# Kernel tuning notes

Hardware: AMD Instinct MI355X
Metric: run time of the kernel (lower is better)

The kernel has to match this reference:

```python
import jax, jax.numpy as jnp
import numpy as np

B, D_IN, D_OUT = 8192, 1024, 1024


def setup_inputs() -> dict:
    key = jax.random.key(0)
    k1, k2 = jax.random.split(key)
    x = jax.random.normal(k1, (B, D_IN), dtype=jnp.float32)
    # Keras add_weight(shape=(3, input_dim, output_dim), initializer='uniform')
    kernel = jax.random.normal(k2, (3, D_IN, D_OUT), dtype=jnp.float32) * 0.05
    return {"x": x, "kernel": kernel}


def reference(x, kernel):
    # x: (B, D). Layer does expand_dims(axis=1) -> (B, 1, D) (seq_len == 1).
    output_dim = kernel.shape[-1]
    xe = x[:, None, :]                                   # (B, 1, D)
    q = jnp.einsum('bsd,do->bso', xe, kernel[0])         # (B, 1, O)
    k = jnp.einsum('bsd,do->bso', xe, kernel[1])         # (B, 1, O)
    v = jnp.einsum('bsd,do->bso', xe, kernel[2])         # (B, 1, O)
    scores = jnp.einsum('bqo,bko->bqk', q, k) / jnp.sqrt(
        jnp.asarray(output_dim, x.dtype))                # (B, 1, 1)
    attn = jax.nn.softmax(scores, axis=-1)
    out = jnp.einsum('bqk,bko->bqo', attn, v)            # (B, 1, O)
    return out
```

## Files before the change

### kernel.cpp

```cpp
#include <hip/hip_runtime.h>
#include <hip/hip_bf16.h>
#include <stdint.h>

#define AS1 __attribute__((address_space(1)))
#define AS3 __attribute__((address_space(3)))

typedef __attribute__((ext_vector_type(8))) short bf16x8_t;
typedef __attribute__((ext_vector_type(4))) float f32x4_t;

#define DDIM 1024
#define WT_ELEMS ((size_t)DDIM * DDIM)

static __device__ inline ushort f32_to_bf16_rne(float f) {
  union { float f; uint32_t u; } v;
  v.f = f;
  v.u += 0x7FFFu + ((v.u >> 16) & 1u);
  return (ushort)(v.u >> 16);
}

__global__ __launch_bounds__(256) void transpose_w(const float* __restrict__ W,
                                                   ushort* __restrict__ Wt) {
  __shared__ float tile[64][65];
  const int t  = threadIdx.x;
  const int bk = blockIdx.x;
  const int bn = blockIdx.y;
#pragma unroll
  for (int s = 0; s < 4; ++s) {
    const int slot = (s << 8) + t;
    const int r    = slot >> 4;
    const int c4   = (slot & 15) << 2;
    const float4 v = *(const float4*)(W + (size_t)(bk * 64 + r) * DDIM + bn * 64 + c4);
    tile[r][c4 + 0] = v.x; tile[r][c4 + 1] = v.y;
    tile[r][c4 + 2] = v.z; tile[r][c4 + 3] = v.w;
  }
  __syncthreads();
#pragma unroll
  for (int s = 0; s < 2; ++s) {
    const int slot = (s << 8) + t;
    const int n    = slot >> 3;
    const int k8   = (slot & 7) << 3;
    union { ushort h[8]; uint4 u; } tmp;
#pragma unroll
    for (int j = 0; j < 8; ++j) tmp.h[j] = f32_to_bf16_rne(tile[k8 + j][n]);
    *(uint4*)(Wt + (size_t)(bn * 64 + n) * DDIM + bk * 64 + k8) = tmp.u;
  }
}

__global__ __launch_bounds__(256, 2) void gemm_fa(const float* __restrict__ X,
                                                  const ushort* __restrict__ Wt,
                                                  float* __restrict__ C) {
  __shared__ __align__(16) ushort As[2][128 * 64];
  __shared__ __align__(16) ushort Bs[2][128 * 64];

  const int t    = threadIdx.x;
  const int wave = t >> 6;
  const int lane = t & 63;
  const int m0 = blockIdx.x * 128;
  const int n0 = blockIdx.y * 128;

  const int sr = t >> 3;
  const int gc = t & 7;
  const int sc = gc ^ (sr & 7);
  const int slotA = sc;

  const float*  aB = X  + (size_t)(m0 + sr) * DDIM + (gc << 3);
  const ushort* bB = Wt + (size_t)(n0 + sr) * DDIM + (sc << 3);

  AS3 char* lB = (AS3 char*)&Bs[0][0];
  const int woff = wave << 10;

  const int wr = (wave >> 1) << 6;
  const int wc = (wave & 1) << 6;
  const int fr = lane & 15;
  const int fq = lane >> 4;

  f32x4_t acc[4][4] = {};

  float4 av[8];

  auto loadA = [&](int kt) {
    const float* a = aB + kt;
#pragma unroll
    for (int j = 0; j < 4; ++j) {
      av[2 * j + 0] = *(const float4*)(a + (size_t)(j << 5) * DDIM);
      av[2 * j + 1] = *(const float4*)(a + (size_t)(j << 5) * DDIM + 4);
    }
  };

  auto issueB = [&](int kt, int p) {
    const ushort* b = bB + kt;
    AS3 char* dB = lB + (p << 14) + woff;
#pragma unroll
    for (int j = 0; j < 4; ++j) {
      __builtin_amdgcn_global_load_lds((const AS1 void*)(b + (size_t)(j << 5) * DDIM),
                                       (AS3 void*)(dB + (j << 12)), 16, 0, 0);
    }
  };

  auto writeA = [&](int pn) {
#pragma unroll
    for (int j = 0; j < 4; ++j) {
      const float4 u0 = av[2 * j + 0];
      const float4 u1 = av[2 * j + 1];
      uint4 w;
      asm("v_cvt_pk_bf16_f32 %0, %1, %2" : "=v"(w.x) : "v"(u0.x), "v"(u0.y));
      asm("v_cvt_pk_bf16_f32 %0, %1, %2" : "=v"(w.y) : "v"(u0.z), "v"(u0.w));
      asm("v_cvt_pk_bf16_f32 %0, %1, %2" : "=v"(w.z) : "v"(u1.x), "v"(u1.y));
      asm("v_cvt_pk_bf16_f32 %0, %1, %2" : "=v"(w.w) : "v"(u1.z), "v"(u1.w));
      const int r = sr + (j << 5);
      *(uint4*)&As[pn][(r << 6) + (slotA << 3)] = w;
    }
  };

  auto compute = [&](int p) {
    const ushort* Ab = &As[p][0];
    const ushort* Bb = &Bs[p][0];
#pragma unroll
    for (int ks = 0; ks < 2; ++ks) {
      const int kc = (ks << 2) + fq;
      bf16x8_t af[4], bfr[4];
#pragma unroll
      for (int mi = 0; mi < 4; ++mi) {
        const int r = wr + (mi << 4) + fr;
        af[mi] = *(const bf16x8_t*)&Ab[(r << 6) + ((kc ^ (r & 7)) << 3)];
      }
#pragma unroll
      for (int ni = 0; ni < 4; ++ni) {
        const int r = wc + (ni << 4) + fr;
        bfr[ni] = *(const bf16x8_t*)&Bb[(r << 6) + ((kc ^ (r & 7)) << 3)];
      }
#pragma unroll
      for (int mi = 0; mi < 4; ++mi)
#pragma unroll
        for (int ni = 0; ni < 4; ++ni)
          acc[mi][ni] = __builtin_amdgcn_mfma_f32_16x16x32_bf16(af[mi], bfr[ni], acc[mi][ni], 0, 0, 0);
    }
  };

  loadA(0);
  issueB(0, 0);
  writeA(0);
  asm volatile("s_waitcnt vmcnt(0) lgkmcnt(0)\n\ts_barrier" ::: "memory");

  for (int i = 0; i < 16; ++i) {
    const int p = i & 1;
    if (i < 15) {
      loadA((i + 1) << 6);
      issueB((i + 1) << 6, p ^ 1);
      asm volatile("s_waitcnt vmcnt(12)\n\ts_barrier" ::: "memory");
    } else {
      asm volatile("s_waitcnt vmcnt(0)\n\ts_barrier" ::: "memory");
    }

    compute(p);

    if (i < 15) {
      writeA(p ^ 1);
      asm volatile("s_waitcnt lgkmcnt(0)\n\ts_barrier" ::: "memory");
    }
  }

#pragma unroll
  for (int mi = 0; mi < 4; ++mi) {
#pragma unroll
    for (int r = 0; r < 4; ++r) {
      const int row = m0 + wr + (mi << 4) + (fq << 2) + r;
      float* crow = C + (size_t)row * DDIM + n0 + wc + fr;
#pragma unroll
      for (int ni = 0; ni < 4; ++ni)
        crow[ni << 4] = acc[mi][ni][r];
    }
  }
}

extern "C" void kernel_launch(void* const* d_in, const int* in_sizes, int n_in,
                              void* d_out, int out_size, void* d_ws, size_t ws_size,
                              hipStream_t stream) {
  const float* x    = (const float*)d_in[0];
  const float* kern = (const float*)d_in[1];
  const float* W = kern + (size_t)2 * DDIM * DDIM;
  ushort* Wt = (ushort*)d_ws;
  const int M = in_sizes[0] / DDIM;

  transpose_w<<<dim3(DDIM / 64, DDIM / 64), 256, 0, stream>>>(W, Wt);
  gemm_fa<<<dim3(M / 128, DDIM / 128), 256, 0, stream>>>(x, Wt, (float*)d_out);
}
```

Measured before the change: 114.4 us.

## Prefetch X tiles two K-steps ahead using double register buffers

Splits the fp32 X register staging into two alternating register buffers and unrolls the main loop by two, so the global loads for X are issued two K-tiles ahead while B is still loaded one tile ahead through the async LDS path. The aim is to hide more global-load latency for the fp32 activations behind the MFMA compute. The cost is roughly 32 extra VGPRs per thread, which may hurt occupancy under the 2-blocks-per-SM launch bound, plus more complex hand-written vmcnt wait counts that must line up with the issue order.

```diff
diff --git a/kernel.cpp b/kernel.cpp
--- a/kernel.cpp
+++ b/kernel.cpp
@@ -9,7 +9,6 @@
 typedef __attribute__((ext_vector_type(4))) float f32x4_t;
 
 #define DDIM 1024
-#define WT_ELEMS ((size_t)DDIM * DDIM)
 
 static __device__ inline ushort f32_to_bf16_rne(float f) {
   union { float f; uint32_t u; } v;
@@ -46,9 +45,9 @@
   }
 }
 
-__global__ __launch_bounds__(256, 2) void gemm_fa(const float* __restrict__ X,
-                                                  const ushort* __restrict__ Wt,
-                                                  float* __restrict__ C) {
+__global__ __launch_bounds__(256, 2) void gemm_fa2(const float* __restrict__ X,
+                                                   const ushort* __restrict__ Wt,
+                                                   float* __restrict__ C) {
   __shared__ __align__(16) ushort As[2][128 * 64];
   __shared__ __align__(16) ushort Bs[2][128 * 64];
 
@@ -76,14 +75,22 @@
 
   f32x4_t acc[4][4] = {};
 
-  float4 av[8];
-
-  auto loadA = [&](int kt) {
+  float4 av0[8], av1[8];
+
+  auto loadA0 = [&](int kt) {
     const float* a = aB + kt;
 #pragma unroll
     for (int j = 0; j < 4; ++j) {
-      av[2 * j + 0] = *(const float4*)(a + (size_t)(j << 5) * DDIM);
-      av[2 * j + 1] = *(const float4*)(a + (size_t)(j << 5) * DDIM + 4);
+      av0[2 * j + 0] = *(const float4*)(a + (size_t)(j << 5) * DDIM);
+      av0[2 * j + 1] = *(const float4*)(a + (size_t)(j << 5) * DDIM + 4);
+    }
+  };
+  auto loadA1 = [&](int kt) {
+    const float* a = aB + kt;
+#pragma unroll
+    for (int j = 0; j < 4; ++j) {
+      av1[2 * j + 0] = *(const float4*)(a + (size_t)(j << 5) * DDIM);
+      av1[2 * j + 1] = *(const float4*)(a + (size_t)(j << 5) * DDIM + 4);
     }
   };
 
@@ -97,11 +104,11 @@
     }
   };
 
-  auto writeA = [&](int pn) {
-#pragma unroll
-    for (int j = 0; j < 4; ++j) {
-      const float4 u0 = av[2 * j + 0];
-      const float4 u1 = av[2 * j + 1];
+  auto writeA0 = [&](int pn) {
+#pragma unroll
+    for (int j = 0; j < 4; ++j) {
+      const float4 u0 = av0[2 * j + 0];
+      const float4 u1 = av0[2 * j + 1];
       uint4 w;
       asm("v_cvt_pk_bf16_f32 %0, %1, %2" : "=v"(w.x) : "v"(u0.x), "v"(u0.y));
       asm("v_cvt_pk_bf16_f32 %0, %1, %2" : "=v"(w.y) : "v"(u0.z), "v"(u0.w));
@@ -111,6 +118,20 @@
       *(uint4*)&As[pn][(r << 6) + (slotA << 3)] = w;
     }
   };
+  auto writeA1 = [&](int pn) {
+#pragma unroll
+    for (int j = 0; j < 4; ++j) {
+      const float4 u0 = av1[2 * j + 0];
+      const float4 u1 = av1[2 * j + 1];
+      uint4 w;
+      asm("v_cvt_pk_bf16_f32 %0, %1, %2" : "=v"(w.x) : "v"(u0.x), "v"(u0.y));
+      asm("v_cvt_pk_bf16_f32 %0, %1, %2" : "=v"(w.y) : "v"(u0.z), "v"(u0.w));
+      asm("v_cvt_pk_bf16_f32 %0, %1, %2" : "=v"(w.z) : "v"(u1.x), "v"(u1.y));
+      asm("v_cvt_pk_bf16_f32 %0, %1, %2" : "=v"(w.w) : "v"(u1.z), "v"(u1.w));
+      const int r = sr + (j << 5);
+      *(uint4*)&As[pn][(r << 6) + (slotA << 3)] = w;
+    }
+  };
 
   auto compute = [&](int p) {
     const ushort* Ab = &As[p][0];
@@ -137,28 +158,35 @@
     }
   };
 
-  loadA(0);
+  loadA0(0);
   issueB(0, 0);
-  writeA(0);
-  asm volatile("s_waitcnt vmcnt(0) lgkmcnt(0)\n\ts_barrier" ::: "memory");
-
-  for (int i = 0; i < 16; ++i) {
-    const int p = i & 1;
-    if (i < 15) {
-      loadA((i + 1) << 6);
-      issueB((i + 1) << 6, p ^ 1);
-      asm volatile("s_waitcnt vmcnt(12)\n\ts_barrier" ::: "memory");
-    } else {
-      asm volatile("s_waitcnt vmcnt(0)\n\ts_barrier" ::: "memory");
-    }
-
-    compute(p);
-
-    if (i < 15) {
-      writeA(p ^ 1);
-      asm volatile("s_waitcnt lgkmcnt(0)\n\ts_barrier" ::: "memory");
-    }
-  }
+  loadA1(1 << 6);
+  writeA0(0);
+  asm volatile("s_waitcnt vmcnt(8) lgkmcnt(0)\n\ts_barrier" ::: "memory");
+
+  for (int ii = 0; ii < 7; ++ii) {
+    const int i0 = ii << 1;
+    loadA0((i0 + 2) << 6);
+    issueB((i0 + 1) << 6, 1);
+    asm volatile("s_waitcnt vmcnt(12)\n\ts_barrier" ::: "memory");
+    compute(0);
+    writeA1(1);
+    asm volatile("s_waitcnt lgkmcnt(0)\n\ts_barrier" ::: "memory");
+    loadA1((i0 + 3) << 6);
+    issueB((i0 + 2) << 6, 0);
+    asm volatile("s_waitcnt vmcnt(12)\n\ts_barrier" ::: "memory");
+    compute(1);
+    writeA0(0);
+    asm volatile("s_waitcnt lgkmcnt(0)\n\ts_barrier" ::: "memory");
+  }
+
+  issueB(15 << 6, 1);
+  asm volatile("s_waitcnt vmcnt(4)\n\ts_barrier" ::: "memory");
+  compute(0);
+  writeA1(1);
+  asm volatile("s_waitcnt lgkmcnt(0)\n\ts_barrier" ::: "memory");
+  asm volatile("s_waitcnt vmcnt(0)\n\ts_barrier" ::: "memory");
+  compute(1);
 
 #pragma unroll
   for (int mi = 0; mi < 4; ++mi) {
@@ -183,5 +211,5 @@
   const int M = in_sizes[0] / DDIM;
 
   transpose_w<<<dim3(DDIM / 64, DDIM / 64), 256, 0, stream>>>(W, Wt);
-  gemm_fa<<<dim3(M / 128, DDIM / 128), 256, 0, stream>>>(x, Wt, (float*)d_out);
-}
+  gemm_fa2<<<dim3(M / 128, DDIM / 128), 256, 0, stream>>>(x, Wt, (float*)d_out);
+}
```

New measurement: 114.9 us. No clear change (+0.5%).
